# Kernel optimization log

Hardware: AMD Instinct MI355X
Metric: run time of the kernel (lower is better)

Reference implementation:

```python
import jax, jax.numpy as jnp
import numpy as np

B, S = 128, 64          # batch, sequence length (cities)
H = 128                 # hidden size
STATIC, DYNAMIC = 2, 2  # static/dynamic feature channels


def setup_inputs() -> dict:
    key = jax.random.key(0)
    ks = jax.random.split(key, 16)
    g = lambda k, shape: (jax.random.normal(k, shape, dtype=jnp.float32) * 0.1)
    return {
        "static": jax.random.normal(ks[0], (B, STATIC, S), dtype=jnp.float32),
        "dynamic": jax.random.uniform(ks[1], (B, DYNAMIC, S), dtype=jnp.float32),
        "x0": jnp.zeros((STATIC,), jnp.float32),           # learned initial decoder input
        "static_w": g(ks[2], (H, STATIC)),  "static_b": g(ks[3], (H,)),
        "dynamic_w": g(ks[4], (H, DYNAMIC)), "dynamic_b": g(ks[5], (H,)),
        "decoder_w": g(ks[6], (H, STATIC)), "decoder_b": g(ks[7], (H,)),
        "gru_wih": g(ks[8], (3 * H, H)), "gru_whh": g(ks[9], (3 * H, H)),
        "gru_bih": g(ks[10], (3 * H,)), "gru_bhh": g(ks[11], (3 * H,)),
        "attn_v": g(ks[12], (H,)), "attn_W": g(ks[13], (H, 3 * H)),
        "ptr_v": g(ks[14], (H,)),  "ptr_W": g(ks[15], (H, 2 * H)),
    }


def _forward(static, dynamic, x0, static_w, static_b, dynamic_w, dynamic_b,
             decoder_w, decoder_b, gru_wih, gru_whh, gru_bih, gru_bhh,
             attn_v, attn_W, ptr_v, ptr_W):
    Bsz, in_size, seq = static.shape
    # Conv1d with kernel_size=1 == pointwise channel mixing
    conv = lambda w, b, x: jnp.einsum('oi,bis->bos', w, x) + b[None, :, None]
    static_h = conv(static_w, static_b, static)      # [B,H,S]
    dynamic_h = conv(dynamic_w, dynamic_b, dynamic)  # [B,H,S]

    def gru_cell(x, h):
        # torch nn.GRU gate order: r, z, n
        gi = x @ gru_wih.T + gru_bih
        gh = h @ gru_whh.T + gru_bhh
        i_r, i_z, i_n = jnp.split(gi, 3, axis=1)
        h_r, h_z, h_n = jnp.split(gh, 3, axis=1)
        r = jax.nn.sigmoid(i_r + h_r)
        z = jax.nn.sigmoid(i_z + h_z)
        n = jnp.tanh(i_n + r * h_n)
        return (1.0 - z) * n + z * h

    def step(carry, _):
        dec_in, h = carry                                   # [B,in,1], [B,H]
        dec_h = conv(decoder_w, decoder_b, dec_in)[:, :, 0]  # [B,H]
        h_new = gru_cell(dec_h, h)                           # rnn_out == last_hh (1 layer)
        rnn_out = h_new
        # encoder attention over cities
        hid = jnp.concatenate(
            [static_h, dynamic_h,
             jnp.broadcast_to(rnn_out[:, :, None], static_h.shape)], axis=1)  # [B,3H,S]
        e = jnp.tanh(jnp.einsum('hk,bks->bhs', attn_W, hid))
        attns = jax.nn.softmax(jnp.einsum('h,bhs->bs', attn_v, e), axis=1)    # [B,S]
        context = jnp.einsum('bs,bhs->bh', attns, static_h)                   # [B,H]
        energy = jnp.concatenate(
            [static_h, jnp.broadcast_to(context[:, :, None], static_h.shape)], axis=1)
        logits = jnp.einsum('h,bhs->bs', ptr_v,
                            jnp.tanh(jnp.einsum('hk,bks->bhs', ptr_W, energy)))
        # mask_fn is None -> mask stays all ones -> mask.log() == 0
        logp_all = jax.nn.log_softmax(logits, axis=1)
        ptr = jnp.argmax(logp_all, axis=1)                  # greedy (eval mode)
        logp = jnp.take_along_axis(logp_all, ptr[:, None], axis=1)[:, 0]
        idx = jnp.broadcast_to(ptr[:, None, None], (Bsz, in_size, 1))
        new_in = jax.lax.stop_gradient(jnp.take_along_axis(static, idx, axis=2))
        return (new_in, h_new), (ptr, logp)

    dec0 = jnp.broadcast_to(x0[None, :, None], (Bsz, in_size, 1))
    h0 = jnp.zeros((Bsz, static_h.shape[1]), static.dtype)
    _, (ptrs, logps) = jax.lax.scan(step, (dec0, h0), None, length=seq)
    return ptrs.T, logps.T  # tour_idx [B,S] int, tour_logp [B,S] float


def reference(static, dynamic, x0, static_w, static_b, dynamic_w, dynamic_b,
              decoder_w, decoder_b, gru_wih, gru_whh, gru_bih, gru_bhh,
              attn_v, attn_W, ptr_v, ptr_W):
    return _forward(static, dynamic, x0, static_w, static_b, dynamic_w, dynamic_b,
                    decoder_w, decoder_b, gru_wih, gru_whh, gru_bih, gru_bhh,
                    attn_v, attn_W, ptr_v, ptr_W)
```

## Files before the change

### kernel.cpp

```cpp
#include <hip/hip_runtime.h>
#include <math.h>


#define K1  1.44269504088896340736f
#define K2  2.88539008177792681472f
#define LN2 0.69314718055994530942f

#define WS_M     0
#define WS_C     768
#define WS_PREA  1152
#define WS_PREP  (WS_PREA + 128*8192)
#define WS_Q     (WS_PREP + 128*8192)

template <int CTRL>
__device__ __forceinline__ float dppf(float x) {
  int xi = __builtin_bit_cast(int, x);
  return __builtin_bit_cast(float,
      __builtin_amdgcn_update_dpp(xi, xi, CTRL, 0xF, 0xF, false));
}
__device__ __forceinline__ float sum4(float x) {
  x += dppf<0xB1>(x); x += dppf<0x4E>(x); return x;
}
__device__ __forceinline__ float sum8(float x) {
  x += dppf<0xB1>(x); x += dppf<0x4E>(x); x += dppf<0x141>(x); return x;
}
__device__ __forceinline__ float sum16(float x) {
  x += dppf<0xB1>(x); x += dppf<0x4E>(x); x += dppf<0x141>(x); x += dppf<0x128>(x);
  return x;
}
__device__ __forceinline__ float sum64(float x) {
  x = sum16(x); x += __shfl_xor(x, 16); x += __shfl_xor(x, 32); return x;
}
__device__ __forceinline__ float max64(float x) {
  x = fmaxf(x, dppf<0xB1>(x)); x = fmaxf(x, dppf<0x4E>(x));
  x = fmaxf(x, dppf<0x141>(x)); x = fmaxf(x, dppf<0x128>(x));
  x = fmaxf(x, __shfl_xor(x, 16)); x = fmaxf(x, __shfl_xor(x, 32)); return x;
}
#define RCP(x)  __builtin_amdgcn_rcpf(x)
#define EXP2(x) __builtin_amdgcn_exp2f(x)

__device__ __forceinline__ void bar_lds() {
  asm volatile("s_waitcnt lgkmcnt(0)" ::: "memory");
  __builtin_amdgcn_s_barrier();
  asm volatile("" ::: "memory");
}

__device__ __forceinline__ int rot8(int p) {
  return (p & 56) | ((p + (p >> 3)) & 7);
}

__global__ __launch_bounds__(256) void prep_small(
    const float* __restrict__ wih, const float* __restrict__ decw,
    const float* __restrict__ decb, const float* __restrict__ bih,
    float* __restrict__ ws) {
  int gid = blockIdx.x * 256 + threadIdx.x;
  if (gid < 384) {
    float m0 = 0.f, m1 = 0.f, cc = 0.f;
    for (int k = 0; k < 128; ++k) {
      float w = wih[gid * 128 + k];
      m0 += w * decw[k * 2 + 0];
      m1 += w * decw[k * 2 + 1];
      cc += w * decb[k];
    }
    ws[WS_M + gid * 2 + 0] = m0;
    ws[WS_M + gid * 2 + 1] = m1;
    ws[WS_C + gid] = cc + bih[gid];
  }
}

__global__ __launch_bounds__(256) void prep_big(
    const float* __restrict__ statics, const float* __restrict__ dynamics,
    const float* __restrict__ sw, const float* __restrict__ sb,
    const float* __restrict__ dw, const float* __restrict__ db,
    const float* __restrict__ attn_W, const float* __restrict__ ptr_W,
    float* __restrict__ ws) {
  __shared__ __align__(16) float sh[128 * 64];
  __shared__ __align__(16) float dh[128 * 64];
  __shared__ float st[128];
  __shared__ float dy[128];
  int b = blockIdx.x >> 3;
  int hq = blockIdx.x & 7;
  int t = threadIdx.x;
  if (t < 128) st[t] = statics[b * 128 + t];
  else         dy[t - 128] = dynamics[b * 128 + (t - 128)];
  __syncthreads();
  for (int e = t; e < 8192; e += 256) {
    int h = e >> 6, s = e & 63;
    sh[e] = sw[h * 2 + 0] * st[s] + sw[h * 2 + 1] * st[64 + s] + sb[h];
    dh[e] = dw[h * 2 + 0] * dy[s] + dw[h * 2 + 1] * dy[64 + s] + db[h];
  }
  __syncthreads();
  int hh = hq * 16 + (t >> 4);
  int s0 = (t & 15) * 4;
  float4 pA = {0, 0, 0, 0}, pP = {0, 0, 0, 0}, qq = {0, 0, 0, 0};
  for (int k = 0; k < 128; ++k) {
    float4 sv = *(const float4*)&sh[k * 64 + s0];
    float4 dv = *(const float4*)&dh[k * 64 + s0];
    float w1 = attn_W[hh * 384 + k];
    float w2 = attn_W[hh * 384 + 128 + k];
    float p1 = ptr_W[hh * 256 + k];
    float p2 = ptr_W[hh * 256 + 128 + k];
    pA.x += w1 * sv.x + w2 * dv.x;  pA.y += w1 * sv.y + w2 * dv.y;
    pA.z += w1 * sv.z + w2 * dv.z;  pA.w += w1 * sv.w + w2 * dv.w;
    pP.x += p1 * sv.x;  pP.y += p1 * sv.y;  pP.z += p1 * sv.z;  pP.w += p1 * sv.w;
    qq.x += p2 * sv.x;  qq.y += p2 * sv.y;  qq.z += p2 * sv.z;  qq.w += p2 * sv.w;
  }
  float4 eA, eP;
  eA.x = exp2f(K2 * pA.x); eA.y = exp2f(K2 * pA.y);
  eA.z = exp2f(K2 * pA.z); eA.w = exp2f(K2 * pA.w);
  eP.x = exp2f(K2 * pP.x); eP.y = exp2f(K2 * pP.y);
  eP.z = exp2f(K2 * pP.z); eP.w = exp2f(K2 * pP.w);
  int o = b * 8192 + hh * 64 + s0;
  *(float4*)&ws[WS_PREA + o] = eA;
  *(float4*)&ws[WS_PREP + o] = eP;
  *(float4*)&ws[WS_Q + o]    = qq;
}

__global__ __launch_bounds__(512)
__attribute__((amdgpu_waves_per_eu(2)))
void drl4tsp_main(
    const float* __restrict__ statics, const float* __restrict__ x0,
    const float* __restrict__ whh, const float* __restrict__ attn_W,
    const float* __restrict__ bhh_g, const float* __restrict__ attn_v,
    const float* __restrict__ ptr_v, const float* __restrict__ ws,
    float* __restrict__ out) {
  __shared__ float4 W3s4[128 * 32];
  __shared__ float4 EAT4[64 * 32];
  __shared__ float4 EPT4[64 * 32];
  __shared__ float4 uav3[64];
  __shared__ float4 uav2[64];
  __shared__ float4 gp4[128 * 3];
  __shared__ __align__(16) float hp[144];
  __shared__ __align__(16) float attns[64];
  __shared__ float a_lds[64];
  __shared__ float l_lds[64];
  __shared__ float stt[128];
  __shared__ float outbuf[128];

  const int b    = blockIdx.x;
  const int t    = threadIdx.x;
  const int lane = t & 63;
  const int g    = t >> 2;
  const int q    = t & 3;
  const int s    = t >> 3;
  const int hg   = t & 7;

  float wr0[32], wr1[32], wr2[32];
#pragma unroll
  for (int kk = 0; kk < 8; ++kk) {
    float4 a = *(const float4*)(whh + g * 128         + kk * 16 + q * 4);
    float4 c = *(const float4*)(whh + (128 + g) * 128 + kk * 16 + q * 4);
    float4 d = *(const float4*)(whh + (256 + g) * 128 + kk * 16 + q * 4);
    wr0[4*kk] = a.x; wr0[4*kk+1] = a.y; wr0[4*kk+2] = a.z; wr0[4*kk+3] = a.w;
    wr1[4*kk] = c.x; wr1[4*kk+1] = c.y; wr1[4*kk+2] = c.z; wr1[4*kk+3] = c.w;
    wr2[4*kk] = d.x; wr2[4*kk+1] = d.y; wr2[4*kk+2] = d.z; wr2[4*kk+3] = d.w;
  }
  float qr[16];
  {
    const float4* pq = (const float4*)(ws + WS_Q + b * 8192 + g * 64 + q * 16);
#pragma unroll
    for (int i = 0; i < 4; ++i) {
      float4 v = pq[i];
      qr[4*i] = v.x; qr[4*i+1] = v.y; qr[4*i+2] = v.z; qr[4*i+3] = v.w;
    }
  }

  {
    const float4* src = (const float4*)(attn_W + g * 384 + 256);
#pragma unroll
    for (int kk = 0; kk < 8; ++kk) {
      int j = q * 8 + kk;
      W3s4[g * 32 + ((j + g) & 31)] = src[j];
    }
  }
  for (int e = t; e < 8192; e += 512) {
    int h = e >> 6, sE = e & 63;
    int rg = ((h >> 2) + sE) & 31;
    ((float*)EAT4)[sE * 128 + rg * 4 + (h & 3)] = ws[WS_PREA + b * 8192 + e];
    ((float*)EPT4)[sE * 128 + rg * 4 + (h & 3)] = ws[WS_PREP + b * 8192 + e];
  }
  if (t < 128) {
    int h = t;
    int rg = rot8(h >> 1);
    ((float*)uav3)[rg * 4 + (h & 1) * 2 + 1] = 2.0f * attn_v[h];
    ((float*)uav2)[rg * 4 + (h & 1) * 2 + 1] = 2.0f * ptr_v[h];
    stt[h] = statics[b * 128 + h];
    const float* Mm = ws + WS_M;
    const float* Cc = ws + WS_C;
    float cR = Cc[h] + bhh_g[h];
    float cZ = Cc[128 + h] + bhh_g[128 + h];
    gp4[h*3 + 0] = float4{Mm[h*2], Mm[h*2+1], cR, Mm[(128+h)*2]};
    gp4[h*3 + 1] = float4{Mm[(128+h)*2+1], cZ, Mm[(256+h)*2], Mm[(256+h)*2+1]};
    gp4[h*3 + 2] = float4{Cc[256+h], bhh_g[256+h], 0.f, 0.f};
  }
  __syncthreads();

  float hreg = 0.f, ghr = 0.f, ghz = 0.f, ghn = 0.f;
  float d0 = x0[0], d1 = x0[1];

  for (int step = 0; step < 64; ++step) {
    {
      float4 v0 = gp4[g*3], v1 = gp4[g*3+1], v2 = gp4[g*3+2];
      float r = RCP(1.f + EXP2(-K1 * (v0.x*d0 + v0.y*d1 + v0.z + ghr)));
      float z = RCP(1.f + EXP2(-K1 * (v0.w*d0 + v1.x*d1 + v1.y + ghz)));
      float xn = v1.z*d0 + v1.w*d1 + v2.x + r * (ghn + v2.y);
      float n = 1.f - 2.f * RCP(EXP2(K2 * xn) + 1.f);
      hreg = (1.f - z) * n + z * hreg;
      if (q == 0) hp[(g >> 5) * 36 + (g & 31)] = hreg;
    }
    bar_lds();
    {
      float u3a = 0.f, u3b = 0.f;
#pragma unroll
      for (int kk = 0; kk < 8; ++kk) {
        float4 hv = *(const float4*)&hp[(kk >> 1) * 36 + (kk & 1) * 16 + q * 4];
        float4 wv = W3s4[g * 32 + ((kk * 4 + q + g) & 31)];
        float d2 = wv.x*hv.x + wv.y*hv.y + wv.z*hv.z + wv.w*hv.w;
        if (kk & 1) u3b += d2; else u3a += d2;
      }
      float u3 = sum4(u3a + u3b);
      if (q == 0)
        ((float*)uav3)[rot8(g >> 1) * 4 + (g & 1) * 2] = EXP2(K2 * u3);
    }
    bar_lds();
    float sr = 0.f, sz = 0.f, sn = 0.f;
    {
      float acc0 = 0.f, acc1 = 0.f;
#pragma unroll
      for (int ii = 0; ii < 4; ++ii) {
        float4 ea = EAT4[s * 32 + ((hg * 4 + ii + s) & 31)];
        int p0 = hg * 8 + 2 * ii;
        float4 ua = uav3[(p0 & 56) | ((p0 + hg) & 7)];
        float4 ub = uav3[((p0+1) & 56) | ((p0 + 1 + hg) & 7)];
        float x1 = ea.x * ua.x + 1.f, y1 = ea.y * ua.z + 1.f;
        acc0 += (ua.y * y1 + ua.w * x1) * RCP(x1 * y1);
        float x2 = ea.z * ub.x + 1.f, y2 = ea.w * ub.z + 1.f;
        acc1 += (ub.y * y2 + ub.w * x2) * RCP(x2 * y2);
      }
#pragma unroll
      for (int kk = 0; kk < 4; ++kk) {
        float4 hv = *(const float4*)&hp[(kk >> 1) * 36 + (kk & 1) * 16 + q * 4];
        int k = kk * 4;
        sr += wr0[k]*hv.x + wr0[k+1]*hv.y + wr0[k+2]*hv.z + wr0[k+3]*hv.w;
        sz += wr1[k]*hv.x + wr1[k+1]*hv.y + wr1[k+2]*hv.z + wr1[k+3]*hv.w;
        sn += wr2[k]*hv.x + wr2[k+1]*hv.y + wr2[k+2]*hv.z + wr2[k+3]*hv.w;
      }
      float acc = sum8(acc0 + acc1);
      if (hg == 0) a_lds[s] = -acc;
    }
    bar_lds();
    float4 ep0, ep1, ep2, ep3;
    {
      float a = a_lds[lane];
      ep0 = EPT4[s * 32 + ((hg * 4 + 0 + s) & 31)];
      ep1 = EPT4[s * 32 + ((hg * 4 + 1 + s) & 31)];
      ep2 = EPT4[s * 32 + ((hg * 4 + 2 + s) & 31)];
      ep3 = EPT4[s * 32 + ((hg * 4 + 3 + s) & 31)];
      float e = EXP2(K1 * a);
      attns[lane] = e;
#pragma unroll
      for (int kk = 4; kk < 8; ++kk) {
        float4 hv = *(const float4*)&hp[(kk >> 1) * 36 + (kk & 1) * 16 + q * 4];
        int k = kk * 4;
        sr += wr0[k]*hv.x + wr0[k+1]*hv.y + wr0[k+2]*hv.z + wr0[k+3]*hv.w;
        sz += wr1[k]*hv.x + wr1[k+1]*hv.y + wr1[k+2]*hv.z + wr1[k+3]*hv.w;
        sn += wr2[k]*hv.x + wr2[k+1]*hv.y + wr2[k+2]*hv.z + wr2[k+3]*hv.w;
      }
      float sum = sum64(e);
      float p = 0.f;
#pragma unroll
      for (int ii = 0; ii < 4; ++ii) {
        float4 av = *(const float4*)&attns[q * 16 + ii * 4];
        p += qr[4*ii]*av.x + qr[4*ii+1]*av.y + qr[4*ii+2]*av.z + qr[4*ii+3]*av.w;
      }
      p *= RCP(sum);
      p = sum4(p);
      if (q == 0)
        ((float*)uav2)[rot8(g >> 1) * 4 + (g & 1) * 2] = EXP2(K2 * p);
      ghr = sum4(sr); ghz = sum4(sz); ghn = sum4(sn);
    }
    bar_lds();
    {
      float acc0 = 0.f, acc1 = 0.f;
#pragma unroll
      for (int ii = 0; ii < 4; ++ii) {
        float4 ep = (ii == 0) ? ep0 : (ii == 1) ? ep1 : (ii == 2) ? ep2 : ep3;
        int p0 = hg * 8 + 2 * ii;
        float4 ua = uav2[(p0 & 56) | ((p0 + hg) & 7)];
        float4 ub = uav2[((p0+1) & 56) | ((p0 + 1 + hg) & 7)];
        float x1 = ep.x * ua.x + 1.f, y1 = ep.y * ua.z + 1.f;
        acc0 += (ua.y * y1 + ua.w * x1) * RCP(x1 * y1);
        float x2 = ep.z * ub.x + 1.f, y2 = ep.w * ub.z + 1.f;
        acc1 += (ub.y * y2 + ub.w * x2) * RCP(x2 * y2);
      }
      float acc = sum8(acc0 + acc1);
      if (hg == 0) l_lds[s] = -acc;
    }
    bar_lds();
    {
      float L = l_lds[lane];
      float v = max64(L);
      unsigned long long mk = __ballot(L == v);
      int idx = __builtin_ctzll(mk);
      float e2 = EXP2(K1 * (L - v));
      float s3 = sum64(e2);
      if (t == 0) {
        outbuf[step] = (float)idx;
        outbuf[64 + step] = -LN2 * __builtin_amdgcn_logf(s3);
      }
      d0 = stt[idx];
      d1 = stt[64 + idx];
    }
  }
  bar_lds();
  if (t < 64)        out[b * 64 + t]         = outbuf[t];
  else if (t < 128)  out[8192 + b * 64 + (t - 64)] = outbuf[t];
}

extern "C" void kernel_launch(void* const* d_in, const int* in_sizes, int n_in,
                              void* d_out, int out_size, void* d_ws, size_t ws_size,
                              hipStream_t stream) {
  const float* statics  = (const float*)d_in[0];
  const float* dynamics = (const float*)d_in[1];
  const float* x0       = (const float*)d_in[2];
  const float* sw       = (const float*)d_in[3];
  const float* sb       = (const float*)d_in[4];
  const float* dw       = (const float*)d_in[5];
  const float* db       = (const float*)d_in[6];
  const float* decw     = (const float*)d_in[7];
  const float* decb     = (const float*)d_in[8];
  const float* wih      = (const float*)d_in[9];
  const float* whh      = (const float*)d_in[10];
  const float* bih      = (const float*)d_in[11];
  const float* bhh      = (const float*)d_in[12];
  const float* attn_v   = (const float*)d_in[13];
  const float* attn_W   = (const float*)d_in[14];
  const float* ptr_v    = (const float*)d_in[15];
  const float* ptr_W    = (const float*)d_in[16];
  float* ws  = (float*)d_ws;
  float* out = (float*)d_out;

  hipLaunchKernelGGL(prep_small, dim3(2), dim3(256), 0, stream,
                     wih, decw, decb, bih, ws);
  hipLaunchKernelGGL(prep_big, dim3(1024), dim3(256), 0, stream,
                     statics, dynamics, sw, sb, dw, db, attn_W, ptr_W, ws);
  hipLaunchKernelGGL(drl4tsp_main, dim3(128), dim3(512), 0, stream,
                     statics, x0, whh, attn_W, bhh, attn_v, ptr_v, ws, out);
}
```

Before: 205.4 us.

## Defer log-softmax normalizer out of the serial decode loop and use DPP row reductions

The per-step log-sum-exp used for the chosen pointer's log-probability is removed from the sequential 64-step loop. Each step's logits are stored in a 16 KB LDS history buffer, and the normalizers are computed in parallel across all 8 waves after the loop. Wave-wide sum and max now use DPP row_shr/row_bcast patterns plus a readlane broadcast instead of ds_swizzle-based shfl_xor. This shortens the serial critical path per step but adds LDS usage, which may affect occupancy.

New measurement: 202.8 us. About the same (-1.2%).

```diff
diff --git a/kernel.cpp b/kernel.cpp
--- a/kernel.cpp
+++ b/kernel.cpp
@@ -13,28 +13,37 @@
 #define WS_Q     (WS_PREP + 128*8192)
 
 template <int CTRL>
-__device__ __forceinline__ float dppf(float x) {
+__device__ __forceinline__ float dppk(float x) {
   int xi = __builtin_bit_cast(int, x);
   return __builtin_bit_cast(float,
       __builtin_amdgcn_update_dpp(xi, xi, CTRL, 0xF, 0xF, false));
 }
+template <int CTRL>
+__device__ __forceinline__ float dppz(float x) {
+  int xi = __builtin_bit_cast(int, x);
+  return __builtin_bit_cast(float,
+      __builtin_amdgcn_update_dpp(0, xi, CTRL, 0xF, 0xF, true));
+}
+__device__ __forceinline__ float bcastf(float x, int lane) {
+  return __builtin_bit_cast(float,
+      __builtin_amdgcn_readlane(__builtin_bit_cast(int, x), lane));
+}
 __device__ __forceinline__ float sum4(float x) {
-  x += dppf<0xB1>(x); x += dppf<0x4E>(x); return x;
+  x += dppk<0xB1>(x); x += dppk<0x4E>(x); return x;
 }
 __device__ __forceinline__ float sum8(float x) {
-  x += dppf<0xB1>(x); x += dppf<0x4E>(x); x += dppf<0x141>(x); return x;
-}
-__device__ __forceinline__ float sum16(float x) {
-  x += dppf<0xB1>(x); x += dppf<0x4E>(x); x += dppf<0x141>(x); x += dppf<0x128>(x);
-  return x;
-}
-__device__ __forceinline__ float sum64(float x) {
-  x = sum16(x); x += __shfl_xor(x, 16); x += __shfl_xor(x, 32); return x;
-}
-__device__ __forceinline__ float max64(float x) {
-  x = fmaxf(x, dppf<0xB1>(x)); x = fmaxf(x, dppf<0x4E>(x));
-  x = fmaxf(x, dppf<0x141>(x)); x = fmaxf(x, dppf<0x128>(x));
-  x = fmaxf(x, __shfl_xor(x, 16)); x = fmaxf(x, __shfl_xor(x, 32)); return x;
+  x += dppk<0xB1>(x); x += dppk<0x4E>(x); x += dppk<0x141>(x); return x;
+}
+__device__ __forceinline__ float wsum64(float x) {
+  x += dppz<0x111>(x); x += dppz<0x112>(x); x += dppz<0x114>(x);
+  x += dppz<0x118>(x); x += dppz<0x142>(x); x += dppz<0x143>(x);
+  return bcastf(x, 63);
+}
+__device__ __forceinline__ float wmax64(float x) {
+  x = fmaxf(x, dppk<0x111>(x)); x = fmaxf(x, dppk<0x112>(x));
+  x = fmaxf(x, dppk<0x114>(x)); x = fmaxf(x, dppk<0x118>(x));
+  x = fmaxf(x, dppk<0x142>(x)); x = fmaxf(x, dppk<0x143>(x));
+  return bcastf(x, 63);
 }
 #define RCP(x)  __builtin_amdgcn_rcpf(x)
 #define EXP2(x) __builtin_amdgcn_exp2f(x)
@@ -135,7 +144,8 @@
   __shared__ float a_lds[64];
   __shared__ float l_lds[64];
   __shared__ float stt[128];
-  __shared__ float outbuf[128];
+  __shared__ float outbuf[64];
+  __shared__ float Lhist[4096];
 
   const int b    = blockIdx.x;
   const int t    = threadIdx.x;
@@ -266,7 +276,7 @@
         sz += wr1[k]*hv.x + wr1[k+1]*hv.y + wr1[k+2]*hv.z + wr1[k+3]*hv.w;
         sn += wr2[k]*hv.x + wr2[k+1]*hv.y + wr2[k+2]*hv.z + wr2[k+3]*hv.w;
       }
-      float sum = sum64(e);
+      float sum = wsum64(e);
       float p = 0.f;
 #pragma unroll
       for (int ii = 0; ii < 4; ++ii) {
@@ -299,22 +309,29 @@
     bar_lds();
     {
       float L = l_lds[lane];
-      float v = max64(L);
+      float v = wmax64(L);
       unsigned long long mk = __ballot(L == v);
       int idx = __builtin_ctzll(mk);
-      float e2 = EXP2(K1 * (L - v));
-      float s3 = sum64(e2);
-      if (t == 0) {
-        outbuf[step] = (float)idx;
-        outbuf[64 + step] = -LN2 * __builtin_amdgcn_logf(s3);
-      }
+      if (t < 64) Lhist[step * 64 + t] = L;
+      if (t == 0) outbuf[step] = (float)idx;
       d0 = stt[idx];
       d1 = stt[64 + idx];
     }
   }
   bar_lds();
-  if (t < 64)        out[b * 64 + t]         = outbuf[t];
-  else if (t < 128)  out[8192 + b * 64 + (t - 64)] = outbuf[t];
+  {
+    int wv = t >> 6;
+    for (int st = wv; st < 64; st += 8) {
+      float L = Lhist[st * 64 + lane];
+      float v = wmax64(L);
+      float e2 = EXP2(K1 * (L - v));
+      float s3 = wsum64(e2);
+      if (lane == 0)
+        out[8192 + b * 64 + st] = -LN2 * __builtin_amdgcn_logf(s3);
+      if (lane == 1)
+        out[b * 64 + st] = outbuf[st];
+    }
+  }
 }
 
 extern "C" void kernel_launch(void* const* d_in, const int* in_sizes, int n_in,
```
